# Kernel tuning notes

Measured on AMD Instinct MI355X. Metric: run time of the kernel, lower is better.

The kernel has to match this reference:

```python
import jax, jax.numpy as jnp
import numpy as np

B, S, IN = 8, 1024, 64
D, F, H, L = 512, 2048, 8, 6
HD = D // H
EPS = 1e-5
GATE_TEMP = 1.0


def _rmsnorm(x, scale):
    return x * scale * jax.lax.rsqrt(jnp.mean(x * x, axis=-1, keepdims=True) + EPS)


def _sinusoidal_pe(seq_len, d_model):
    pos = np.arange(seq_len)[:, None].astype(np.float32)
    div = np.exp(np.arange(0, d_model, 2).astype(np.float32) * (-np.log(10000.0) / d_model))
    pe = np.zeros((seq_len, d_model), dtype=np.float32)
    pe[:, 0::2] = np.sin(pos * div)
    pe[:, 1::2] = np.cos(pos * div)
    return jnp.asarray(pe)


def setup_inputs() -> dict:
    key = jax.random.key(0)
    ks = jax.random.split(key, 12)
    s = 0.02
    return {
        "src": jax.random.normal(ks[0], (B, S, IN), jnp.float32),
        "in_w": jax.random.normal(ks[1], (IN, D), jnp.float32) * s,
        "in_b": jnp.zeros((D,), jnp.float32),
        "Wq": jax.random.normal(ks[2], (L, D, D), jnp.float32) * s,
        "Wk": jax.random.normal(ks[3], (L, D, D), jnp.float32) * s,
        "Wv": jax.random.normal(ks[4], (L, D, D), jnp.float32) * s,
        "Wo": jax.random.normal(ks[5], (L, D, D), jnp.float32) * s,
        "bq": jnp.zeros((L, D), jnp.float32),
        "bk": jnp.zeros((L, D), jnp.float32),
        "bv": jnp.zeros((L, D), jnp.float32),
        "bo": jnp.zeros((L, D), jnp.float32),
        "n1": jnp.ones((L, D), jnp.float32),
        "n2": jnp.ones((L, D), jnp.float32),
        "Wg": jax.random.normal(ks[6], (L, D, F), jnp.float32) * s,
        "Wu": jax.random.normal(ks[7], (L, D, F), jnp.float32) * s,
        "Wd": jax.random.normal(ks[8], (L, F, D), jnp.float32) * s,
        "gate_w": jax.random.normal(ks[9], (L, D), jnp.float32) * s,
        "gate_b": jnp.full((L,), 2.0, jnp.float32),  # LayerGate init_bias=2.0
        "final_scale": jnp.ones((D,), jnp.float32),
    }


def reference(src, in_w, in_b, Wq, Wk, Wv, Wo, bq, bk, bv, bo, n1, n2,
              Wg, Wu, Wd, gate_w, gate_b, final_scale):
    b, s, _ = src.shape
    x = src @ in_w + in_b                      # input_adapter: [B,S,D]
    x = x + _sinusoidal_pe(s, D)               # PositionalEncoding, scale=1.0
    inv_sqrt_hd = 1.0 / jnp.sqrt(jnp.asarray(HD, x.dtype))
    for i in range(L):
        # --- pre-norm self-attention block ---
        h = _rmsnorm(x, n1[i])
        q = (h @ Wq[i] + bq[i]).reshape(b, s, H, HD)
        k = (h @ Wk[i] + bk[i]).reshape(b, s, H, HD)
        v = (h @ Wv[i] + bv[i]).reshape(b, s, H, HD)
        scores = jnp.einsum("bqhd,bkhd->bhqk", q, k) * inv_sqrt_hd
        attn = jax.nn.softmax(scores, axis=-1)
        ctx = jnp.einsum("bhqk,bkhd->bqhd", attn, v).reshape(b, s, D)
        y = x + (ctx @ Wo[i] + bo[i])
        # --- pre-norm SwiGLU FFN block ---
        h2 = _rmsnorm(y, n2[i])
        y = y + (jax.nn.silu(h2 @ Wg[i]) * (h2 @ Wu[i])) @ Wd[i]
        # --- LayerGate: seq-mode hard skip with straight-through estimator ---
        pooled = jnp.mean(x, axis=1)                           # gate on layer input [B,D]
        p = jax.nn.sigmoid((pooled @ gate_w[i] + gate_b[i]) / GATE_TEMP)  # [B]
        hard = (p > 0.5).astype(x.dtype)
        g = hard + p - jax.lax.stop_gradient(p)
        x = g[:, None, None] * y + (1.0 - g)[:, None, None] * x
    return _rmsnorm(x, final_scale)
```

## Files before the change

kernel.cpp:

```cpp
#include <hip/hip_runtime.h>


typedef unsigned short u16;
typedef __attribute__((ext_vector_type(8))) __bf16 bf16x8;
typedef __attribute__((ext_vector_type(4))) float f32x4;
typedef __attribute__((ext_vector_type(16))) float f32x16;
typedef __attribute__((ext_vector_type(8))) unsigned short u16x8;

#define DEV __device__ __forceinline__

DEV u16 f2bf(float f) {
  unsigned u = __builtin_bit_cast(unsigned, f);
  u += 0x7fffu + ((u >> 16) & 1u);
  return (u16)(u >> 16);
}
DEV float bf2f(u16 h) { return __builtin_bit_cast(float, ((unsigned)h) << 16); }

DEV void gload16(const void* g, void* l) {
  __builtin_amdgcn_global_load_lds(
      (__attribute__((address_space(1))) void*)g,
      (__attribute__((address_space(3))) void*)l, 16, 0, 0);
}

DEV void xcd_map(int& bx, int& by) {
  const int nx = gridDim.x, ny = gridDim.y;
  const int orig = by * nx + bx;
  const int cpx = (nx * ny) >> 3;
  const int swz = (orig & 7) * cpx + (orig >> 3);
  by = swz / nx; bx = swz - by * nx;
}

__global__ __launch_bounds__(256) void transpose_all_kernel(
    const float* __restrict__ Wq, const float* __restrict__ Wk,
    const float* __restrict__ Wv, const float* __restrict__ Wo,
    const float* __restrict__ Wg, const float* __restrict__ Wu,
    const float* __restrict__ Wd,
    u16* __restrict__ WqkvT, u16* __restrict__ WoT, u16* __restrict__ WgT,
    u16* __restrict__ WuT, u16* __restrict__ WdT)
{
  const int l = blockIdx.y;
  const int idx = blockIdx.x;
  const float* src; u16* dst; int N, bx, by;
  if (idx < 1024) {
    const int w = idx >> 8, t = idx & 255;
    bx = t & 15; by = t >> 4; N = 512;
    const size_t lo = (size_t)l * 262144;
    if (w == 0)      { src = Wq + lo; dst = WqkvT + (size_t)l * 786432; }
    else if (w == 1) { src = Wk + lo; dst = WqkvT + (size_t)l * 786432 + 262144; }
    else if (w == 2) { src = Wv + lo; dst = WqkvT + (size_t)l * 786432 + 524288; }
    else             { src = Wo + lo; dst = WoT + lo; }
  } else if (idx < 2048) {
    const int t = idx - 1024; bx = t & 63; by = t >> 6; N = 2048;
    src = Wg + (size_t)l * 1048576; dst = WgT + (size_t)l * 1048576;
  } else if (idx < 3072) {
    const int t = idx - 2048; bx = t & 63; by = t >> 6; N = 2048;
    src = Wu + (size_t)l * 1048576; dst = WuT + (size_t)l * 1048576;
  } else {
    const int t = idx - 3072; bx = t & 15; by = t >> 4; N = 512;
    src = Wd + (size_t)l * 1048576; dst = WdT + (size_t)l * 1048576;
  }
  const int K = (idx >= 3072) ? 2048 : 512;
  __shared__ float tl[32][33];
  const int n0 = bx * 32, k0 = by * 32;
  const int tx = threadIdx.x & 31, ty = threadIdx.x >> 5;
#pragma unroll
  for (int i = 0; i < 4; ++i)
    tl[ty + i * 8][tx] = src[(size_t)(k0 + ty + i * 8) * N + n0 + tx];
  __syncthreads();
#pragma unroll
  for (int i = 0; i < 4; ++i)
    dst[(size_t)(n0 + ty + i * 8) * K + k0 + tx] = f2bf(tl[tx][ty + i * 8]);
}

__global__ void biaspack_kernel(const float* __restrict__ bq,
                                const float* __restrict__ bk,
                                const float* __restrict__ bv,
                                float* __restrict__ out)
{
  const int l = blockIdx.x;
  for (int c = threadIdx.x; c < 1536; c += 256) {
    float v = (c < 512) ? bq[l * 512 + c]
            : (c < 1024) ? bk[l * 512 + c - 512]
                         : bv[l * 512 + c - 1024];
    out[l * 1536 + c] = v;
  }
}

__global__ __launch_bounds__(256) void adapter_kernel(
    const float* __restrict__ src, const float* __restrict__ w,
    const float* __restrict__ bias, float* __restrict__ x)
{
  __shared__ float srow[8][64];
  const int m0 = blockIdx.y * 8;
  const int n = blockIdx.x * 256 + threadIdx.x;
  for (int i = threadIdx.x; i < 512; i += 256)
    srow[i >> 6][i & 63] = src[(size_t)m0 * 64 + i];
  __syncthreads();
  float acc[8];
#pragma unroll
  for (int r = 0; r < 8; ++r) acc[r] = bias[n];
  for (int k = 0; k < 64; ++k) {
    const float wv = w[(size_t)k * 512 + n];
#pragma unroll
    for (int r = 0; r < 8; ++r) acc[r] = fmaf(srow[r][k], wv, acc[r]);
  }
  const int i2 = n & ~1;
  const float freq = expf((float)i2 * (-9.210340371976184f / 512.0f));
#pragma unroll
  for (int r = 0; r < 8; ++r) {
    const int pos = (m0 + r) & 1023;
    const float ang = (float)pos * freq;
    acc[r] += (n & 1) ? cosf(ang) : sinf(ang);
    x[(size_t)(m0 + r) * 512 + n] = acc[r];
  }
}

template <bool BF16OUT>
__global__ __launch_bounds__(256) void rmsnorm_kernel(
    const float* __restrict__ x, const float* __restrict__ scale,
    u16* __restrict__ outb, float* __restrict__ outf)
{
  const int wave = threadIdx.x >> 6, lane = threadIdx.x & 63;
  const size_t row = (size_t)blockIdx.x * 4 + wave;
  const f32x4* xr = (const f32x4*)(x + row * 512);
  f32x4 a = xr[lane * 2], c = xr[lane * 2 + 1];
  float ss = a[0]*a[0] + a[1]*a[1] + a[2]*a[2] + a[3]*a[3]
           + c[0]*c[0] + c[1]*c[1] + c[2]*c[2] + c[3]*c[3];
#pragma unroll
  for (int d = 1; d < 64; d <<= 1) ss += __shfl_xor(ss, d);
  const float r = rsqrtf(ss * (1.0f / 512.0f) + 1e-5f);
  const f32x4* sr = (const f32x4*)scale;
  f32x4 s1 = sr[lane * 2], s2 = sr[lane * 2 + 1];
  if (BF16OUT) {
    u16x8 ov;
    ov[0] = f2bf(a[0] * s1[0] * r); ov[1] = f2bf(a[1] * s1[1] * r);
    ov[2] = f2bf(a[2] * s1[2] * r); ov[3] = f2bf(a[3] * s1[3] * r);
    ov[4] = f2bf(c[0] * s2[0] * r); ov[5] = f2bf(c[1] * s2[1] * r);
    ov[6] = f2bf(c[2] * s2[2] * r); ov[7] = f2bf(c[3] * s2[3] * r);
    *(u16x8*)(outb + row * 512 + lane * 8) = ov;
  } else {
    f32x4 o1, o2;
    o1[0] = a[0]*s1[0]*r; o1[1] = a[1]*s1[1]*r; o1[2] = a[2]*s1[2]*r; o1[3] = a[3]*s1[3]*r;
    o2[0] = c[0]*s2[0]*r; o2[1] = c[1]*s2[1]*r; o2[2] = c[2]*s2[2]*r; o2[3] = c[3]*s2[3]*r;
    f32x4* orow = (f32x4*)(outf + row * 512);
    orow[lane * 2] = o1; orow[lane * 2 + 1] = o2;
  }
}

template <int MODE, int BN>
__global__ __launch_bounds__(256) void gemm_bt(
    const u16* __restrict__ A, const u16* __restrict__ Bt,
    const float* __restrict__ bias, const float* __restrict__ resf,
    float* __restrict__ outf, u16* __restrict__ outb,
    const float* __restrict__ gatep, const float* __restrict__ gbias,
    int layer, int M, int N, int K)
{
  constexpr int NI = BN / 32;
  __shared__ __align__(16) u16 lA[128 * 64];
  __shared__ __align__(16) u16 lB[BN * 64];
  const int tid = threadIdx.x;
  const int wave = tid >> 6, lane = tid & 63;
  const int lr = lane & 15, lg = lane >> 4;
  int bx = blockIdx.x, by = blockIdx.y;
  xcd_map(bx, by);
  const int m0 = by << 7, n0 = bx * BN;
  const int wr = wave >> 1, wc = wave & 1;
  if (MODE == 4) {
    __shared__ float gfl;
    if (tid < 64) {
      float v = gatep[(m0 >> 10) * 64 + tid];
#pragma unroll
      for (int d = 1; d < 64; d <<= 1) v += __shfl_xor(v, d);
      if (tid == 0) gfl = (v / 1024.0f + gbias[layer] > 0.0f) ? 1.0f : 0.0f;
    }
    __syncthreads();
    if (gfl == 0.0f) return;
  }
  f32x4 acc[4][NI] = {};
  for (int kt = 0; kt < K; kt += 64) {
    __syncthreads();
#pragma unroll
    for (int i = 0; i < 4; ++i) {
      const int c = i * 256 + tid;
      const int row = c >> 3, kc = ((c & 7) ^ (row & 7)) << 3;
      gload16(A + (size_t)(m0 + row) * K + kt + kc,
              lA + (size_t)(i * 256 + wave * 64) * 8);
    }
#pragma unroll
    for (int i = 0; i < BN / 32; ++i) {
      const int c = i * 256 + tid;
      const int row = c >> 3, kc = ((c & 7) ^ (row & 7)) << 3;
      gload16(Bt + (size_t)(n0 + row) * K + kt + kc,
              lB + (size_t)(i * 256 + wave * 64) * 8);
    }
    __syncthreads();
    bf16x8 af[2][4], bfr[2][NI];
#pragma unroll
    for (int kk = 0; kk < 2; ++kk) {
#pragma unroll
      for (int mi = 0; mi < 4; ++mi) {
        const int row = wr * 64 + mi * 16 + lr;
        af[kk][mi] = *(const bf16x8*)&lA[row * 64 + (((kk * 4 + lg) ^ (row & 7)) << 3)];
      }
#pragma unroll
      for (int ni = 0; ni < NI; ++ni) {
        const int row = wc * (BN / 2) + ni * 16 + lr;
        bfr[kk][ni] = *(const bf16x8*)&lB[row * 64 + (((kk * 4 + lg) ^ (row & 7)) << 3)];
      }
    }
#pragma unroll
    for (int kk = 0; kk < 2; ++kk)
#pragma unroll
      for (int mi = 0; mi < 4; ++mi)
#pragma unroll
        for (int ni = 0; ni < NI; ++ni)
          acc[mi][ni] = __builtin_amdgcn_mfma_f32_16x16x32_bf16(
              af[kk][mi], bfr[kk][ni], acc[mi][ni], 0, 0, 0);
  }
#pragma unroll
  for (int mi = 0; mi < 4; ++mi) {
#pragma unroll
    for (int ni = 0; ni < NI; ++ni) {
      const int col = n0 + wc * (BN / 2) + ni * 16 + lr;
      const float bs = (MODE == 0 || MODE == 1) ? bias[col] : 0.0f;
#pragma unroll
      for (int j = 0; j < 4; ++j) {
        const int row = m0 + wr * 64 + mi * 16 + lg * 4 + j;
        const size_t idx = (size_t)row * N + col;
        float v = acc[mi][ni][j] + bs;
        if (MODE == 0) {
          if (col < 512) v *= 0.125f;
          outb[idx] = f2bf(v);
        } else {
          outf[idx] = v + resf[idx];
        }
      }
    }
  }
}

__global__ __launch_bounds__(256) void gemm_glu(
    const u16* __restrict__ A, const u16* __restrict__ Bg,
    const u16* __restrict__ Bu, u16* __restrict__ outT)
{
  constexpr int K = 512, N = 2048;
  __shared__ __align__(16) u16 lA[128 * 64];
  __shared__ __align__(16) u16 lG[64 * 64];
  __shared__ __align__(16) u16 lU[64 * 64];
  const int tid = threadIdx.x;
  const int wave = tid >> 6, lane = tid & 63;
  const int lr = lane & 15, lg = lane >> 4;
  int bx = blockIdx.x, by = blockIdx.y;
  xcd_map(bx, by);
  const int m0 = by << 7, n0 = bx << 6;
  const int wr = wave >> 1, wc = wave & 1;
  f32x4 ag[4][2] = {}, au[4][2] = {};
  for (int kt = 0; kt < K; kt += 64) {
    __syncthreads();
#pragma unroll
    for (int i = 0; i < 4; ++i) {
      const int c = i * 256 + tid;
      const int row = c >> 3, kc = ((c & 7) ^ (row & 7)) << 3;
      gload16(A + (size_t)(m0 + row) * K + kt + kc,
              lA + (size_t)(i * 256 + wave * 64) * 8);
    }
#pragma unroll
    for (int i = 0; i < 2; ++i) {
      const int c = i * 256 + tid;
      const int row = c >> 3, kc = ((c & 7) ^ (row & 7)) << 3;
      const size_t dst = (size_t)(i * 256 + wave * 64) * 8;
      gload16(Bg + (size_t)(n0 + row) * K + kt + kc, lG + dst);
      gload16(Bu + (size_t)(n0 + row) * K + kt + kc, lU + dst);
    }
    __syncthreads();
    bf16x8 af[2][4], gf[2][2], uf[2][2];
#pragma unroll
    for (int kk = 0; kk < 2; ++kk) {
#pragma unroll
      for (int mi = 0; mi < 4; ++mi) {
        const int row = wr * 64 + mi * 16 + lr;
        af[kk][mi] = *(const bf16x8*)&lA[row * 64 + (((kk * 4 + lg) ^ (row & 7)) << 3)];
      }
#pragma unroll
      for (int ni = 0; ni < 2; ++ni) {
        const int row = wc * 32 + ni * 16 + lr;
        const int off = row * 64 + (((kk * 4 + lg) ^ (row & 7)) << 3);
        gf[kk][ni] = *(const bf16x8*)&lG[off];
        uf[kk][ni] = *(const bf16x8*)&lU[off];
      }
    }
#pragma unroll
    for (int kk = 0; kk < 2; ++kk)
#pragma unroll
      for (int mi = 0; mi < 4; ++mi)
#pragma unroll
        for (int ni = 0; ni < 2; ++ni) {
          ag[mi][ni] = __builtin_amdgcn_mfma_f32_16x16x32_bf16(
              af[kk][mi], gf[kk][ni], ag[mi][ni], 0, 0, 0);
          au[mi][ni] = __builtin_amdgcn_mfma_f32_16x16x32_bf16(
              af[kk][mi], uf[kk][ni], au[mi][ni], 0, 0, 0);
        }
  }
#pragma unroll
  for (int mi = 0; mi < 4; ++mi) {
#pragma unroll
    for (int ni = 0; ni < 2; ++ni) {
      const int col = n0 + wc * 32 + ni * 16 + lr;
#pragma unroll
      for (int j = 0; j < 4; ++j) {
        const int row = m0 + wr * 64 + mi * 16 + lg * 4 + j;
        const float g = ag[mi][ni][j];
        const float sg = g / (1.0f + __expf(-g));
        outT[(size_t)row * N + col] = f2bf(sg * au[mi][ni][j]);
      }
    }
  }
}

__global__ __launch_bounds__(256) void attn_kernel(
    const u16* __restrict__ qkv, u16* __restrict__ ctx)
{
  constexpr int LD = 1536;
  const int qblk = blockIdx.x, bh = blockIdx.y;
  const int b = bh >> 3, h = bh & 7;
  const int tid = threadIdx.x, wave = tid >> 6, lane = tid & 63;
  const int l31 = lane & 31, half = lane >> 5;
  const size_t rowb = (size_t)b * 1024;
  const int q0 = qblk * 128 + wave * 32;

  __shared__ __align__(16) u16 Ksh[2][64 * 64];
  __shared__ __align__(16) u16 Vsh[2][64 * 64];
  __shared__ __align__(16) u16 PL[4][32 * 64];
  __shared__ float rl_lds[4][32];

  const u16* qrow = qkv + (rowb + q0 + l31) * LD + h * 64;
  bf16x8 qf[4];
#pragma unroll
  for (int c = 0; c < 4; ++c)
    qf[c] = *(const bf16x8*)(qrow + c * 16 + half * 8);

  const int krow0 = tid >> 3;
  const int kch0 = (tid & 7) ^ (krow0 & 7);
  const int vm = tid >> 3, vd0 = (tid & 7) * 8;
  const int vswz = (vm >> 2) ^ (tid & 7);
  char* vbase0 = (char*)Vsh + (vswz << 4) + ((vm & 3) << 2);
  const u16* kg = qkv + rowb * LD + 512 + h * 64;
  const u16* vg = qkv + (rowb + 2 * vm) * LD + 1024 + h * 64 + vd0;

  f32x16 o0 = {}, o1 = {};
  float l_acc = 0.0f;

  gload16(kg + (size_t)(0 + krow0) * LD + kch0 * 8, Ksh[0] + wave * 512);
  gload16(kg + (size_t)(32 + krow0) * LD + kch0 * 8, Ksh[0] + 2048 + wave * 512);
  {
    u16x8 va = *(const u16x8*)vg;
    u16x8 vb = *(const u16x8*)(vg + LD);
#pragma unroll
    for (int j = 0; j < 8; ++j) {
      const unsigned w = (unsigned)va[j] | ((unsigned)vb[j] << 16);
      *(unsigned*)(vbase0 + (vd0 + j) * 128) = w;
    }
  }
  __syncthreads();

  for (int t = 0; t < 16; ++t) {
    const int cur = t & 1, nxt = cur ^ 1;
    const int k0n = (t + 1) * 64;
    u16x8 va2, vb2;
    if (t < 15) {
      gload16(kg + (size_t)(k0n + krow0) * LD + kch0 * 8,
              Ksh[nxt] + wave * 512);
      gload16(kg + (size_t)(k0n + 32 + krow0) * LD + kch0 * 8,
              Ksh[nxt] + 2048 + wave * 512);
      va2 = *(const u16x8*)(vg + (size_t)k0n * LD);
      vb2 = *(const u16x8*)(vg + (size_t)k0n * LD + LD);
    }

    const char* kshb = (const char*)Ksh[cur];
    const char* vshb = (const char*)Vsh[cur];

    f32x16 s0 = {}, s1 = {};
#pragma unroll
    for (int c = 0; c < 4; ++c) {
      {
        const int row = l31;
        bf16x8 kf = *(const bf16x8*)(kshb + row * 128 +
                        ((((c << 1) | half) ^ (row & 7)) << 4));
        s0 = __builtin_amdgcn_mfma_f32_32x32x16_bf16(kf, qf[c], s0, 0, 0, 0);
      }
      {
        const int row = 32 + l31;
        bf16x8 kf = *(const bf16x8*)(kshb + row * 128 +
                        ((((c << 1) | half) ^ (row & 7)) << 4));
        s1 = __builtin_amdgcn_mfma_f32_32x32x16_bf16(kf, qf[c], s1, 0, 0, 0);
      }
    }

    char* plw = (char*)PL[wave];
#pragma unroll
    for (int blk = 0; blk < 2; ++blk) {
      const f32x16 sv = blk ? s1 : s0;
#pragma unroll
      for (int rg = 0; rg < 4; ++rg) {
        const float e0 = __expf(fminf(sv[rg * 4 + 0], 60.0f));
        const float e1 = __expf(fminf(sv[rg * 4 + 1], 60.0f));
        const float e2 = __expf(fminf(sv[rg * 4 + 2], 60.0f));
        const float e3 = __expf(fminf(sv[rg * 4 + 3], 60.0f));
        l_acc += (e0 + e1) + (e2 + e3);
        const unsigned lo = (unsigned)f2bf(e0) | ((unsigned)f2bf(e1) << 16);
        const unsigned hi = (unsigned)f2bf(e2) | ((unsigned)f2bf(e3) << 16);
        const int chunk = (rg + 4 * blk) ^ (l31 & 7);
        *(unsigned long long*)(plw + l31 * 128 + (chunk << 4) + half * 8) =
            (unsigned long long)lo | ((unsigned long long)hi << 32);
      }
    }

#pragma unroll
    for (int c = 0; c < 4; ++c) {
      bf16x8 pf = *(const bf16x8*)(plw + l31 * 128 +
                      ((((c << 1) | half) ^ (l31 & 7)) << 4));
      {
        const int row = l31;
        bf16x8 vf = *(const bf16x8*)(vshb + row * 128 +
                        ((((c << 1) | half) ^ (row >> 3)) << 4));
        o0 = __builtin_amdgcn_mfma_f32_32x32x16_bf16(pf, vf, o0, 0, 0, 0);
      }
      {
        const int row = 32 + l31;
        bf16x8 vf = *(const bf16x8*)(vshb + row * 128 +
                        ((((c << 1) | half) ^ (row >> 3)) << 4));
        o1 = __builtin_amdgcn_mfma_f32_32x32x16_bf16(pf, vf, o1, 0, 0, 0);
      }
    }

    if (t < 15) {
      char* vbn = (char*)Vsh[nxt] + (vswz << 4) + ((vm & 3) << 2);
#pragma unroll
      for (int j = 0; j < 8; ++j) {
        const unsigned w = (unsigned)va2[j] | ((unsigned)vb2[j] << 16);
        *(unsigned*)(vbn + (vd0 + j) * 128) = w;
      }
    }
    __syncthreads();
  }

  const float l_tot = l_acc + __shfl_xor(l_acc, 32);
  if (lane < 32) rl_lds[wave][l31] = 1.0f / l_tot;
  __syncthreads();
#pragma unroll
  for (int r = 0; r < 16; ++r) {
    const int q_r = (r & 3) + 8 * (r >> 2) + 4 * half;
    const float rl = rl_lds[wave][q_r];
    const size_t orow = (rowb + q0 + q_r) * 512 + h * 64 + l31;
    ctx[orow] = f2bf(o0[r] * rl);
    ctx[orow + 32] = f2bf(o1[r] * rl);
  }
}

__global__ __launch_bounds__(256) void gate_partial_kernel(
    const float* __restrict__ x, const float* __restrict__ gw,
    float* __restrict__ gp)
{
  const int b = blockIdx.x, chunk = blockIdx.y, tid = threadIdx.x;
  const float* xb = x + (size_t)b * 1024 * 512 + (size_t)chunk * 16 * 512;
  float acc = 0.0f;
#pragma unroll
  for (int k = 0; k < 8; ++k) {
    const int i = tid * 4 + k * 1024;
    f32x4 v = *(const f32x4*)(xb + i);
    f32x4 wv = *(const f32x4*)(gw + (i & 511));
    acc += v[0]*wv[0] + v[1]*wv[1] + v[2]*wv[2] + v[3]*wv[3];
  }
  __shared__ float red[256];
  red[tid] = acc;
  __syncthreads();
  for (int s = 128; s > 32; s >>= 1) {
    if (tid < s) red[tid] += red[tid + s];
    __syncthreads();
  }
  if (tid < 32) {
    float v = red[tid] + red[tid + 32];
#pragma unroll
    for (int d = 1; d < 32; d <<= 1) v += __shfl_xor(v, d);
    if (tid == 0) gp[b * 64 + chunk] = v;
  }
}

extern "C" void kernel_launch(void* const* d_in, const int* in_sizes, int n_in,
                              void* d_out, int out_size, void* d_ws, size_t ws_size,
                              hipStream_t stream)
{
  (void)in_sizes; (void)n_in; (void)out_size; (void)ws_size;
  const float* src  = (const float*)d_in[0];
  const float* in_w = (const float*)d_in[1];
  const float* in_b = (const float*)d_in[2];
  const float* Wq   = (const float*)d_in[3];
  const float* Wk   = (const float*)d_in[4];
  const float* Wv   = (const float*)d_in[5];
  const float* Wo   = (const float*)d_in[6];
  const float* bq   = (const float*)d_in[7];
  const float* bk   = (const float*)d_in[8];
  const float* bv   = (const float*)d_in[9];
  const float* bo   = (const float*)d_in[10];
  const float* n1   = (const float*)d_in[11];
  const float* n2   = (const float*)d_in[12];
  const float* Wg   = (const float*)d_in[13];
  const float* Wu   = (const float*)d_in[14];
  const float* Wd   = (const float*)d_in[15];
  const float* gw   = (const float*)d_in[16];
  const float* gb   = (const float*)d_in[17];
  const float* fs   = (const float*)d_in[18];

  char* ws = (char*)d_ws;
  size_t off = 0;
  auto alloc = [&](size_t bytes) -> void* {
    void* p = ws + off;
    off += (bytes + 255) & ~(size_t)255;
    return p;
  };
  u16*   WqkvT = (u16*)alloc(6ULL * 1536 * 512 * 2);
  u16*   WoT   = (u16*)alloc(6ULL * 512 * 512 * 2);
  u16*   WgT   = (u16*)alloc(6ULL * 2048 * 512 * 2);
  u16*   WuT   = (u16*)alloc(6ULL * 2048 * 512 * 2);
  u16*   WdT   = (u16*)alloc(6ULL * 512 * 2048 * 2);
  float* bqkv  = (float*)alloc(6ULL * 1536 * 4);
  float* x     = (float*)alloc(8192ULL * 512 * 4);
  float* y     = (float*)alloc(8192ULL * 512 * 4);
  u16*   hbuf  = (u16*)alloc(8192ULL * 512 * 2);
  u16*   sA    = (u16*)alloc(8192ULL * 2048 * 2);
  u16*   sB    = (u16*)alloc(8192ULL * 2048 * 2);
  float* gp    = (float*)alloc(512 * 4);

  const dim3 tb(256);
  transpose_all_kernel<<<dim3(4096, 6), tb, 0, stream>>>(
      Wq, Wk, Wv, Wo, Wg, Wu, Wd, WqkvT, WoT, WgT, WuT, WdT);
  biaspack_kernel<<<6, tb, 0, stream>>>(bq, bk, bv, bqkv);
  adapter_kernel<<<dim3(2, 1024), tb, 0, stream>>>(src, in_w, in_b, x);

  for (int l = 0; l < 6; ++l) {
    gate_partial_kernel<<<dim3(8, 64), tb, 0, stream>>>(x, gw + l * 512, gp);
    rmsnorm_kernel<true><<<2048, tb, 0, stream>>>(x, n1 + l * 512, hbuf, nullptr);
    gemm_bt<0, 128><<<dim3(12, 64), tb, 0, stream>>>(
        hbuf, WqkvT + (size_t)l * 1536 * 512, bqkv + l * 1536,
        nullptr, nullptr, sA, nullptr, nullptr, 0, 8192, 1536, 512);
    attn_kernel<<<dim3(8, 64), tb, 0, stream>>>(sA, sB);
    gemm_bt<1, 64><<<dim3(8, 64), tb, 0, stream>>>(
        sB, WoT + (size_t)l * 512 * 512, bo + l * 512,
        x, y, nullptr, nullptr, nullptr, 0, 8192, 512, 512);
    rmsnorm_kernel<true><<<2048, tb, 0, stream>>>(y, n2 + l * 512, hbuf, nullptr);
    gemm_glu<<<dim3(32, 64), tb, 0, stream>>>(
        hbuf, WgT + (size_t)l * 2048 * 512, WuT + (size_t)l * 2048 * 512, sB);
    gemm_bt<4, 64><<<dim3(8, 64), tb, 0, stream>>>(
        sB, WdT + (size_t)l * 512 * 2048, nullptr,
        y, x, nullptr, gp, gb, l, 8192, 512, 2048);
  }
  rmsnorm_kernel<false><<<2048, tb, 0, stream>>>(x, fs, nullptr, (float*)d_out);
}
```

Measured before the change: 1.015 ms.

## Double-buffer LDS tiles in gemm_bt and gemm_glu to overlap loads with MFMA

Both GEMM kernels now hold two LDS buffers per operand and prefetch the next K-tile with global_load_lds while computing on the current one. Each iteration drops to one barrier. The aim is to hide global-to-LDS latency behind the matrix-core work. In exchange, LDS use doubles, which can reduce occupancy. The async LDS loads are also only ordered by the trailing __syncthreads, so correctness relies on that barrier draining the outstanding vmcnt loads.

```diff
diff --git a/kernel.cpp b/kernel.cpp
--- a/kernel.cpp
+++ b/kernel.cpp
@@ -156,8 +156,8 @@
     int layer, int M, int N, int K)
 {
   constexpr int NI = BN / 32;
-  __shared__ __align__(16) u16 lA[128 * 64];
-  __shared__ __align__(16) u16 lB[BN * 64];
+  __shared__ __align__(16) u16 lA[2][128 * 64];
+  __shared__ __align__(16) u16 lB[2][BN * 64];
   const int tid = threadIdx.x;
   const int wave = tid >> 6, lane = tid & 63;
   const int lr = lane & 15, lg = lane >> 4;
@@ -176,36 +176,42 @@
     __syncthreads();
     if (gfl == 0.0f) return;
   }
-  f32x4 acc[4][NI] = {};
-  for (int kt = 0; kt < K; kt += 64) {
-    __syncthreads();
+
+  auto stage = [&](int buf, int kt) {
 #pragma unroll
     for (int i = 0; i < 4; ++i) {
       const int c = i * 256 + tid;
       const int row = c >> 3, kc = ((c & 7) ^ (row & 7)) << 3;
       gload16(A + (size_t)(m0 + row) * K + kt + kc,
-              lA + (size_t)(i * 256 + wave * 64) * 8);
+              lA[buf] + (size_t)(i * 256 + wave * 64) * 8);
     }
 #pragma unroll
     for (int i = 0; i < BN / 32; ++i) {
       const int c = i * 256 + tid;
       const int row = c >> 3, kc = ((c & 7) ^ (row & 7)) << 3;
       gload16(Bt + (size_t)(n0 + row) * K + kt + kc,
-              lB + (size_t)(i * 256 + wave * 64) * 8);
-    }
-    __syncthreads();
+              lB[buf] + (size_t)(i * 256 + wave * 64) * 8);
+    }
+  };
+
+  f32x4 acc[4][NI] = {};
+  stage(0, 0);
+  __syncthreads();
+  int cur = 0;
+  for (int kt = 0; kt < K; kt += 64) {
+    if (kt + 64 < K) stage(cur ^ 1, kt + 64);
     bf16x8 af[2][4], bfr[2][NI];
 #pragma unroll
     for (int kk = 0; kk < 2; ++kk) {
 #pragma unroll
       for (int mi = 0; mi < 4; ++mi) {
         const int row = wr * 64 + mi * 16 + lr;
-        af[kk][mi] = *(const bf16x8*)&lA[row * 64 + (((kk * 4 + lg) ^ (row & 7)) << 3)];
+        af[kk][mi] = *(const bf16x8*)&lA[cur][row * 64 + (((kk * 4 + lg) ^ (row & 7)) << 3)];
       }
 #pragma unroll
       for (int ni = 0; ni < NI; ++ni) {
         const int row = wc * (BN / 2) + ni * 16 + lr;
-        bfr[kk][ni] = *(const bf16x8*)&lB[row * 64 + (((kk * 4 + lg) ^ (row & 7)) << 3)];
+        bfr[kk][ni] = *(const bf16x8*)&lB[cur][row * 64 + (((kk * 4 + lg) ^ (row & 7)) << 3)];
       }
     }
 #pragma unroll
@@ -216,6 +222,8 @@
         for (int ni = 0; ni < NI; ++ni)
           acc[mi][ni] = __builtin_amdgcn_mfma_f32_16x16x32_bf16(
               af[kk][mi], bfr[kk][ni], acc[mi][ni], 0, 0, 0);
+    __syncthreads();
+    cur ^= 1;
   }
 #pragma unroll
   for (int mi = 0; mi < 4; ++mi) {
@@ -244,9 +252,9 @@
     const u16* __restrict__ Bu, u16* __restrict__ outT)
 {
   constexpr int K = 512, N = 2048;
-  __shared__ __align__(16) u16 lA[128 * 64];
-  __shared__ __align__(16) u16 lG[64 * 64];
-  __shared__ __align__(16) u16 lU[64 * 64];
+  __shared__ __align__(16) u16 lA[2][128 * 64];
+  __shared__ __align__(16) u16 lG[2][64 * 64];
+  __shared__ __align__(16) u16 lU[2][64 * 64];
   const int tid = threadIdx.x;
   const int wave = tid >> 6, lane = tid & 63;
   const int lr = lane & 15, lg = lane >> 4;
@@ -254,39 +262,45 @@
   xcd_map(bx, by);
   const int m0 = by << 7, n0 = bx << 6;
   const int wr = wave >> 1, wc = wave & 1;
-  f32x4 ag[4][2] = {}, au[4][2] = {};
-  for (int kt = 0; kt < K; kt += 64) {
-    __syncthreads();
+
+  auto stage = [&](int buf, int kt) {
 #pragma unroll
     for (int i = 0; i < 4; ++i) {
       const int c = i * 256 + tid;
       const int row = c >> 3, kc = ((c & 7) ^ (row & 7)) << 3;
       gload16(A + (size_t)(m0 + row) * K + kt + kc,
-              lA + (size_t)(i * 256 + wave * 64) * 8);
+              lA[buf] + (size_t)(i * 256 + wave * 64) * 8);
     }
 #pragma unroll
     for (int i = 0; i < 2; ++i) {
       const int c = i * 256 + tid;
       const int row = c >> 3, kc = ((c & 7) ^ (row & 7)) << 3;
       const size_t dst = (size_t)(i * 256 + wave * 64) * 8;
-      gload16(Bg + (size_t)(n0 + row) * K + kt + kc, lG + dst);
-      gload16(Bu + (size_t)(n0 + row) * K + kt + kc, lU + dst);
-    }
-    __syncthreads();
+      gload16(Bg + (size_t)(n0 + row) * K + kt + kc, lG[buf] + dst);
+      gload16(Bu + (size_t)(n0 + row) * K + kt + kc, lU[buf] + dst);
+    }
+  };
+
+  f32x4 ag[4][2] = {}, au[4][2] = {};
+  stage(0, 0);
+  __syncthreads();
+  int cur = 0;
+  for (int kt = 0; kt < K; kt += 64) {
+    if (kt + 64 < K) stage(cur ^ 1, kt + 64);
     bf16x8 af[2][4], gf[2][2], uf[2][2];
 #pragma unroll
     for (int kk = 0; kk < 2; ++kk) {
 #pragma unroll
       for (int mi = 0; mi < 4; ++mi) {
         const int row = wr * 64 + mi * 16 + lr;
-        af[kk][mi] = *(const bf16x8*)&lA[row * 64 + (((kk * 4 + lg) ^ (row & 7)) << 3)];
+        af[kk][mi] = *(const bf16x8*)&lA[cur][row * 64 + (((kk * 4 + lg) ^ (row & 7)) << 3)];
       }
 #pragma unroll
       for (int ni = 0; ni < 2; ++ni) {
         const int row = wc * 32 + ni * 16 + lr;
         const int off = row * 64 + (((kk * 4 + lg) ^ (row & 7)) << 3);
-        gf[kk][ni] = *(const bf16x8*)&lG[off];
-        uf[kk][ni] = *(const bf16x8*)&lU[off];
+        gf[kk][ni] = *(const bf16x8*)&lG[cur][off];
+        uf[kk][ni] = *(const bf16x8*)&lU[cur][off];
       }
     }
 #pragma unroll
@@ -300,6 +314,8 @@
           au[mi][ni] = __builtin_amdgcn_mfma_f32_16x16x32_bf16(
               af[kk][mi], uf[kk][ni], au[mi][ni], 0, 0, 0);
         }
+    __syncthreads();
+    cur ^= 1;
   }
 #pragma unroll
   for (int mi = 0; mi < 4; ++mi) {
```

Measured after the change: 1.048 ms. 3.3% more time.
